# Kernel tuning notes

Measured on AMD Instinct MI355X. Metric: run time of the kernel, lower is better.

Reference implementation:

```python
import jax, jax.numpy as jnp
import numpy as np

N = 50000   # nodes
E = 800000  # random edges (self-loops appended inside reference, as PyG GATConv does)
H = 4       # attention heads
LEAKY_SLOPE = 0.2
BN_EPS = 1e-5


def setup_inputs() -> dict:
    key = jax.random.key(0)
    ks = jax.random.split(key, 24)
    inp = {
        "x": jax.random.normal(ks[0], (N, 128), jnp.float32),
        "edge_index": jax.random.randint(ks[1], (2, E), 0, N, dtype=jnp.int64),
    }
    # layer dims: (in, out_per_head); concat -> out width = H*out
    dims = [(128, 64), (256, 64), (256, 32)]
    i = 2
    for l, (fin, c) in enumerate(dims, start=1):
        sc = 1.0 / np.sqrt(fin)
        inp[f"W{l}"] = jax.random.normal(ks[i], (fin, H * c), jnp.float32) * sc; i += 1
        inp[f"a_src{l}"] = jax.random.normal(ks[i], (H, c), jnp.float32) * 0.1; i += 1
        inp[f"a_dst{l}"] = jax.random.normal(ks[i], (H, c), jnp.float32) * 0.1; i += 1
        inp[f"b{l}"] = jnp.zeros((H * c,), jnp.float32)
    # batch norm params for the two non-final layers (width = 64*4 = 256)
    for l in (1, 2):
        inp[f"gamma{l}"] = jnp.ones((256,), jnp.float32)
        inp[f"beta{l}"] = jnp.zeros((256,), jnp.float32)
    return inp


def _gat_layer(x, src, dst, W, a_src, a_dst, b, heads):
    n = x.shape[0]
    h = (x @ W).reshape(n, heads, -1)                      # [N,H,C]
    al_s = jnp.sum(h * a_src, axis=-1)                     # [N,H]
    al_d = jnp.sum(h * a_dst, axis=-1)                     # [N,H]
    e = jax.nn.leaky_relu(al_s[src] + al_d[dst], LEAKY_SLOPE)  # [Etot,H]
    # numerically-stable edge softmax over incoming edges per destination
    m = jax.ops.segment_max(e, dst, num_segments=n)
    e = jnp.exp(e - m[dst])
    s = jax.ops.segment_sum(e, dst, num_segments=n)
    alpha = e / (s[dst] + 1e-16)                           # [Etot,H]
    msg = alpha[:, :, None] * h[src]                       # [Etot,H,C]
    out = jax.ops.segment_sum(msg, dst, num_segments=n)    # [N,H,C]
    out = out.reshape(n, -1) + b
    return jax.nn.relu(out)  # GAT_NET applies relu after conv


def _batch_norm(x, gamma, beta):
    mean = jnp.mean(x, axis=0)
    var = jnp.var(x, axis=0)  # biased, matches torch BN training normalization
    return (x - mean) * jax.lax.rsqrt(var + BN_EPS) * gamma + beta


def reference(x, edge_index, W1, a_src1, a_dst1, b1, gamma1, beta1,
              W2, a_src2, a_dst2, b2, gamma2, beta2,
              W3, a_src3, a_dst3, b3):
    n = x.shape[0]
    loop = jnp.arange(n, dtype=edge_index.dtype)
    src = jnp.concatenate([edge_index[0], loop])  # add self-loops (PyG default)
    dst = jnp.concatenate([edge_index[1], loop])

    h = _gat_layer(x, src, dst, W1, a_src1, a_dst1, b1, H)
    # outer F.relu is a no-op after GAT_NET's internal relu, kept implicitly
    h = _batch_norm(h, gamma1, beta1)

    h = _gat_layer(h, src, dst, W2, a_src2, a_dst2, b2, H)
    h = _batch_norm(h, gamma2, beta2)

    return _gat_layer(h, src, dst, W3, a_src3, a_dst3, b3, H)
```

## Files before the change

kernel.cpp:

```cpp
#include <hip/hip_runtime.h>
#include <hip/hip_bf16.h>

constexpr int NN   = 50000;
constexpr int EE   = 800000;
constexpr int ETOT = EE + NN;
constexpr int NP   = 50048;
constexpr int NBLK = (NN + 255) / 256;
constexpr float SLOPE  = 0.2f;
constexpr float EPS_BN = 1e-5f;

typedef __attribute__((ext_vector_type(8))) short bf16x8;
typedef __attribute__((ext_vector_type(4))) float f32x4;

__device__ inline float bf2f(unsigned short u) {
    union { unsigned int i; float f; } c; c.i = ((unsigned int)u) << 16; return c.f;
}

__device__ inline void gload16(const __hip_bfloat16* g, __hip_bfloat16* l) {
    __builtin_amdgcn_global_load_lds(
        (const __attribute__((address_space(1))) unsigned int*)g,
        (__attribute__((address_space(3))) unsigned int*)l, 16, 0, 0);
}


__global__ __launch_bounds__(256) void count_kernel(const int* __restrict__ ei,
                                                    int* __restrict__ cnt) {
    int j = blockIdx.x * 256 + threadIdx.x;
    if (j >= ETOT) return;
    int dst = (j < EE) ? ei[EE + j] : (j - EE);
    atomicAdd(&cnt[dst], 1);
}

__global__ __launch_bounds__(256) void scanA_kernel(const int* __restrict__ cnt,
                                                    int* __restrict__ off,
                                                    int* __restrict__ bsum) {
    int b = blockIdx.x, t = threadIdx.x;
    int i = b * 256 + t;
    int v = (i < NN) ? cnt[i] : 0;
    int lane = t & 63, w = t >> 6;
    int x = v;
    #pragma unroll
    for (int o = 1; o < 64; o <<= 1) { int y = __shfl_up(x, o); if (lane >= o) x += y; }
    __shared__ int ws[4];
    if (lane == 63) ws[w] = x;
    __syncthreads();
    int wo = 0;
    for (int k = 0; k < w; ++k) wo += ws[k];
    int incl = x + wo;
    if (i < NN) off[i] = incl - v;
    if (t == 255) bsum[b] = incl;
}

__global__ __launch_bounds__(256) void scanB_kernel(const int* __restrict__ bsum,
                                                    int* __restrict__ bexc,
                                                    int* __restrict__ off) {
    int t = threadIdx.x;
    int v = (t < NBLK) ? bsum[t] : 0;
    int lane = t & 63, w = t >> 6;
    int x = v;
    #pragma unroll
    for (int o = 1; o < 64; o <<= 1) { int y = __shfl_up(x, o); if (lane >= o) x += y; }
    __shared__ int ws[4];
    if (lane == 63) ws[w] = x;
    __syncthreads();
    int wo = 0;
    for (int k = 0; k < w; ++k) wo += ws[k];
    int incl = x + wo;
    if (t < NBLK) bexc[t] = incl - v;
    if (t == 255) off[NN] = incl;
}

__global__ __launch_bounds__(256) void scanC_kernel(const int* __restrict__ bexc,
                                                    int* __restrict__ off,
                                                    int* __restrict__ cur) {
    int i = blockIdx.x * 256 + threadIdx.x;
    if (i >= NN) return;
    int v = off[i] + bexc[blockIdx.x];
    off[i] = v;
    cur[i] = v;
}

__global__ __launch_bounds__(256) void fill_kernel(const int* __restrict__ ei,
                                                   int* __restrict__ cursor,
                                                   int* __restrict__ ssrc) {
    int j = blockIdx.x * 256 + threadIdx.x;
    if (j >= ETOT) return;
    int src, dst;
    if (j < EE) { src = ei[j]; dst = ei[EE + j]; }
    else        { src = dst = j - EE; }
    int pos = atomicAdd(&cursor[dst], 1);
    ssrc[pos] = src;
}

__global__ __launch_bounds__(256) void castx_kernel(const float* __restrict__ X,
                                                    __hip_bfloat16* __restrict__ Xbf) {
    long e0 = ((long)blockIdx.x * 256 + threadIdx.x) * 8;
    if (e0 >= (long)NP * 128) return;
    int row = (int)(e0 / 128);
    __hip_bfloat16 o[8];
    if (row < NN) {
        float4 v0 = *reinterpret_cast<const float4*>(X + e0);
        float4 v1 = *reinterpret_cast<const float4*>(X + e0 + 4);
        o[0] = __float2bfloat16(v0.x); o[1] = __float2bfloat16(v0.y);
        o[2] = __float2bfloat16(v0.z); o[3] = __float2bfloat16(v0.w);
        o[4] = __float2bfloat16(v1.x); o[5] = __float2bfloat16(v1.y);
        o[6] = __float2bfloat16(v1.z); o[7] = __float2bfloat16(v1.w);
    } else {
        for (int j = 0; j < 8; ++j) o[j] = __float2bfloat16(0.f);
    }
    *reinterpret_cast<bf16x8*>(Xbf + e0) = *reinterpret_cast<bf16x8*>(o);
}

__global__ __launch_bounds__(256) void castw1_kernel(const float* __restrict__ W,
                                                     __hip_bfloat16* __restrict__ WT) {
    int i = blockIdx.x * 256 + threadIdx.x;
    if (i >= 32768) return;
    int c = i / 128, k = i % 128;
    WT[i] = __float2bfloat16(W[(size_t)k * 256 + c]);
}

template <int FIN, int WOUT>
__global__ __launch_bounds__(FIN) void foldw_kernel(const float* __restrict__ W,
                                                    const float* __restrict__ scale,
                                                    const float* __restrict__ shift,
                                                    __hip_bfloat16* __restrict__ WTp,
                                                    float* __restrict__ bb) {
    int c = blockIdx.x, k = threadIdx.x;
    float w = W[(size_t)k * WOUT + c];
    WTp[(size_t)c * FIN + k] = __float2bfloat16(scale[k] * w);
    float p = shift[k] * w;
    #pragma unroll
    for (int o = 1; o < 64; o <<= 1) p += __shfl_xor(p, o);
    __shared__ float ps[FIN / 64];
    if ((k & 63) == 0) ps[k >> 6] = p;
    __syncthreads();
    if (k == 0) {
        float s = 0.f;
        #pragma unroll
        for (int q = 0; q < FIN / 64; ++q) s += ps[q];
        bb[c] = s;
    }
}

template <int FIN, int WOUT, bool FOLD>
__global__ __launch_bounds__(256) void mgemm_kernel(const __hip_bfloat16* __restrict__ A,
                                                    const __hip_bfloat16* __restrict__ BT,
                                                    const float* __restrict__ bb,
                                                    const float* __restrict__ a_src,
                                                    const float* __restrict__ a_dst,
                                                    __hip_bfloat16* __restrict__ Hbf,
                                                    float* __restrict__ als,
                                                    float* __restrict__ ald) {
    __shared__ __hip_bfloat16 As[128 * 32];
    __shared__ __hip_bfloat16 Bs[128 * 32];
    int t = threadIdx.x;
    int lane = t & 63, w = t >> 6;
    int row0 = blockIdx.x * 128;
    int col0 = blockIdx.y * 128;
    int wr = w >> 1, wc = w & 1;

    f32x4 acc[4][4];
    #pragma unroll
    for (int m = 0; m < 4; ++m)
        #pragma unroll
        for (int n = 0; n < 4; ++n) acc[m][n] = (f32x4){0.f, 0.f, 0.f, 0.f};

    int srow = w * 32 + (lane >> 2);
    int sbc  = (lane & 3) * 8;
    const __hip_bfloat16* gA0 = A  + (size_t)(row0 + srow)      * FIN + sbc;
    const __hip_bfloat16* gA1 = A  + (size_t)(row0 + srow + 16) * FIN + sbc;
    const __hip_bfloat16* gB0 = BT + (size_t)(col0 + srow)      * FIN + sbc;
    const __hip_bfloat16* gB1 = BT + (size_t)(col0 + srow + 16) * FIN + sbc;
    __hip_bfloat16* lA0 = As + w * 1024;
    __hip_bfloat16* lA1 = As + w * 1024 + 512;
    __hip_bfloat16* lB0 = Bs + w * 1024;
    __hip_bfloat16* lB1 = Bs + w * 1024 + 512;

    int rA = (wr * 64 + (lane & 15)) * 32 + (lane >> 4) * 8;
    int rB = (wc * 64 + (lane & 15)) * 32 + (lane >> 4) * 8;

    for (int k0 = 0; k0 < FIN; k0 += 32) {
        gload16(gA0 + k0, lA0);
        gload16(gA1 + k0, lA1);
        gload16(gB0 + k0, lB0);
        gload16(gB1 + k0, lB1);
        __syncthreads();
        bf16x8 af[4], bfr[4];
        #pragma unroll
        for (int m = 0; m < 4; ++m) af[m]  = *reinterpret_cast<const bf16x8*>(As + rA + m * 16 * 32);
        #pragma unroll
        for (int n = 0; n < 4; ++n) bfr[n] = *reinterpret_cast<const bf16x8*>(Bs + rB + n * 16 * 32);
        #pragma unroll
        for (int m = 0; m < 4; ++m)
            #pragma unroll
            for (int n = 0; n < 4; ++n)
                acc[m][n] = __builtin_amdgcn_mfma_f32_16x16x32_bf16(af[m], bfr[n], acc[m][n], 0, 0, 0);
        __syncthreads();
    }

    int cih = lane & 15;

    if constexpr (FOLD) {
        #pragma unroll
        for (int n = 0; n < 4; ++n) {
            float badd = bb[col0 + wc * 64 + n * 16 + cih];
            #pragma unroll
            for (int m = 0; m < 4; ++m)
                #pragma unroll
                for (int j = 0; j < 4; ++j) acc[m][n][j] += badd;
        }
    }

    float asv[4], adv[4];
    int headw = 0;
    if constexpr (WOUT == 256) {
        headw = (col0 >> 6) + wc;
        #pragma unroll
        for (int n = 0; n < 4; ++n) {
            asv[n] = a_src[headw * 64 + n * 16 + cih];
            adv[n] = a_dst[headw * 64 + n * 16 + cih];
        }
    } else {
        #pragma unroll
        for (int n = 0; n < 4; ++n) {
            int hh = wc * 2 + (n >> 1);
            asv[n] = a_src[hh * 32 + (n & 1) * 16 + cih];
            adv[n] = a_dst[hh * 32 + (n & 1) * 16 + cih];
        }
    }

    #pragma unroll
    for (int m = 0; m < 4; ++m) {
        #pragma unroll
        for (int j = 0; j < 4; ++j) {
            int r = row0 + wr * 64 + m * 16 + (lane >> 4) * 4 + j;
            if constexpr (WOUT == 256) {
                float vs = acc[m][0][j] * asv[0] + acc[m][1][j] * asv[1]
                         + acc[m][2][j] * asv[2] + acc[m][3][j] * asv[3];
                float vd = acc[m][0][j] * adv[0] + acc[m][1][j] * adv[1]
                         + acc[m][2][j] * adv[2] + acc[m][3][j] * adv[3];
                #pragma unroll
                for (int o = 1; o < 16; o <<= 1) {
                    vs += __shfl_xor(vs, o);
                    vd += __shfl_xor(vd, o);
                }
                if (cih == 0) {
                    als[(size_t)r * 4 + headw] = vs;
                    ald[(size_t)r * 4 + headw] = vd;
                }
            } else {
                float vs0 = acc[m][0][j] * asv[0] + acc[m][1][j] * asv[1];
                float vs1 = acc[m][2][j] * asv[2] + acc[m][3][j] * asv[3];
                float vd0 = acc[m][0][j] * adv[0] + acc[m][1][j] * adv[1];
                float vd1 = acc[m][2][j] * adv[2] + acc[m][3][j] * adv[3];
                #pragma unroll
                for (int o = 1; o < 16; o <<= 1) {
                    vs0 += __shfl_xor(vs0, o); vs1 += __shfl_xor(vs1, o);
                    vd0 += __shfl_xor(vd0, o); vd1 += __shfl_xor(vd1, o);
                }
                if (cih == 0) {
                    als[(size_t)r * 4 + wc * 2]     = vs0;
                    als[(size_t)r * 4 + wc * 2 + 1] = vs1;
                    ald[(size_t)r * 4 + wc * 2]     = vd0;
                    ald[(size_t)r * 4 + wc * 2 + 1] = vd1;
                }
            }
        }
    }

    #pragma unroll
    for (int n = 0; n < 4; ++n) {
        int c = col0 + wc * 64 + n * 16 + cih;
        #pragma unroll
        for (int m = 0; m < 4; ++m) {
            int r = row0 + wr * 64 + m * 16 + (lane >> 4) * 4;
            #pragma unroll
            for (int j = 0; j < 4; ++j)
                Hbf[(size_t)(r + j) * WOUT + c] = __float2bfloat16(acc[m][n][j]);
        }
    }
}

template <int HC, bool OUTBF>
__global__ __launch_bounds__(256) void attn_kernel(const __hip_bfloat16* __restrict__ Hm,
                                                   const int* __restrict__ off,
                                                   const int* __restrict__ ssrc,
                                                   const float* __restrict__ als,
                                                   const float* __restrict__ ald,
                                                   const float* __restrict__ bias,
                                                   void* __restrict__ Outv) {
    constexpr int CPL = HC / 16;
    int wid  = threadIdx.x >> 6;
    int lane = threadIdx.x & 63;
    int g    = lane >> 4;
    int q    = lane & 15;
    int d    = blockIdx.x * 16 + wid * 4 + g;
    int head = q >> 2;

    int e0 = off[d], e1 = off[d + 1];
    float aldh = ald[(size_t)d * 4 + head];

    float acc[CPL];
    #pragma unroll
    for (int c = 0; c < CPL; ++c) acc[c] = 0.f;
    float den = 0.f;

    int j = e0;
    for (; j + 3 < e1; j += 4) {
        int s0 = ssrc[j], s1 = ssrc[j + 1], s2 = ssrc[j + 2], s3 = ssrc[j + 3];
        float x0 = als[(size_t)s0 * 4 + head] + aldh;
        float x1 = als[(size_t)s1 * 4 + head] + aldh;
        float x2 = als[(size_t)s2 * 4 + head] + aldh;
        float x3 = als[(size_t)s3 * 4 + head] + aldh;
        x0 = (x0 > 0.f) ? x0 : SLOPE * x0;
        x1 = (x1 > 0.f) ? x1 : SLOPE * x1;
        x2 = (x2 > 0.f) ? x2 : SLOPE * x2;
        x3 = (x3 > 0.f) ? x3 : SLOPE * x3;
        float w0 = __expf(x0), w1 = __expf(x1), w2 = __expf(x2), w3 = __expf(x3);
        den += (w0 + w1) + (w2 + w3);
        const __hip_bfloat16* p0 = Hm + (size_t)s0 * HC + q * CPL;
        const __hip_bfloat16* p1 = Hm + (size_t)s1 * HC + q * CPL;
        const __hip_bfloat16* p2 = Hm + (size_t)s2 * HC + q * CPL;
        const __hip_bfloat16* p3 = Hm + (size_t)s3 * HC + q * CPL;
        if constexpr (CPL == 16) {
            bf16x8 a0 = *reinterpret_cast<const bf16x8*>(p0);
            bf16x8 a1 = *reinterpret_cast<const bf16x8*>(p0 + 8);
            bf16x8 b0 = *reinterpret_cast<const bf16x8*>(p1);
            bf16x8 b1 = *reinterpret_cast<const bf16x8*>(p1 + 8);
            bf16x8 c0 = *reinterpret_cast<const bf16x8*>(p2);
            bf16x8 c1 = *reinterpret_cast<const bf16x8*>(p2 + 8);
            bf16x8 d0 = *reinterpret_cast<const bf16x8*>(p3);
            bf16x8 d1 = *reinterpret_cast<const bf16x8*>(p3 + 8);
            #pragma unroll
            for (int c = 0; c < 8; ++c) {
                acc[c]     += w0 * bf2f((unsigned short)a0[c]) + w1 * bf2f((unsigned short)b0[c])
                            + w2 * bf2f((unsigned short)c0[c]) + w3 * bf2f((unsigned short)d0[c]);
                acc[8 + c] += w0 * bf2f((unsigned short)a1[c]) + w1 * bf2f((unsigned short)b1[c])
                            + w2 * bf2f((unsigned short)c1[c]) + w3 * bf2f((unsigned short)d1[c]);
            }
        } else {
            bf16x8 a0 = *reinterpret_cast<const bf16x8*>(p0);
            bf16x8 b0 = *reinterpret_cast<const bf16x8*>(p1);
            bf16x8 c0 = *reinterpret_cast<const bf16x8*>(p2);
            bf16x8 d0 = *reinterpret_cast<const bf16x8*>(p3);
            #pragma unroll
            for (int c = 0; c < 8; ++c)
                acc[c] += w0 * bf2f((unsigned short)a0[c]) + w1 * bf2f((unsigned short)b0[c])
                        + w2 * bf2f((unsigned short)c0[c]) + w3 * bf2f((unsigned short)d0[c]);
        }
    }
    for (; j < e1; ++j) {
        int s0 = ssrc[j];
        float x0 = als[(size_t)s0 * 4 + head] + aldh;
        x0 = (x0 > 0.f) ? x0 : SLOPE * x0;
        float w0 = __expf(x0);
        den += w0;
        const __hip_bfloat16* p0 = Hm + (size_t)s0 * HC + q * CPL;
        if constexpr (CPL == 16) {
            bf16x8 a0 = *reinterpret_cast<const bf16x8*>(p0);
            bf16x8 a1 = *reinterpret_cast<const bf16x8*>(p0 + 8);
            #pragma unroll
            for (int c = 0; c < 8; ++c) {
                acc[c]     += w0 * bf2f((unsigned short)a0[c]);
                acc[8 + c] += w0 * bf2f((unsigned short)a1[c]);
            }
        } else {
            bf16x8 a0 = *reinterpret_cast<const bf16x8*>(p0);
            #pragma unroll
            for (int c = 0; c < 8; ++c) acc[c] += w0 * bf2f((unsigned short)a0[c]);
        }
    }

    float inv = 1.f / (den + 1e-16f);

    float o[CPL];
    #pragma unroll
    for (int c4 = 0; c4 < CPL / 4; ++c4) {
        float4 b4 = *reinterpret_cast<const float4*>(bias + q * CPL + c4 * 4);
        o[c4 * 4 + 0] = fmaxf(acc[c4 * 4 + 0] * inv + b4.x, 0.f);
        o[c4 * 4 + 1] = fmaxf(acc[c4 * 4 + 1] * inv + b4.y, 0.f);
        o[c4 * 4 + 2] = fmaxf(acc[c4 * 4 + 2] * inv + b4.z, 0.f);
        o[c4 * 4 + 3] = fmaxf(acc[c4 * 4 + 3] * inv + b4.w, 0.f);
    }
    if constexpr (OUTBF) {
        __hip_bfloat16 ob[CPL];
        #pragma unroll
        for (int c = 0; c < CPL; ++c) ob[c] = __float2bfloat16(o[c]);
        __hip_bfloat16* op = (__hip_bfloat16*)Outv + (size_t)d * HC + q * CPL;
        #pragma unroll
        for (int c8 = 0; c8 < CPL / 8; ++c8)
            *reinterpret_cast<bf16x8*>(op + c8 * 8) = *reinterpret_cast<bf16x8*>(ob + c8 * 8);
    } else {
        float* op = (float*)Outv + (size_t)d * HC + q * CPL;
        #pragma unroll
        for (int c4 = 0; c4 < CPL / 4; ++c4)
            *reinterpret_cast<float4*>(op + c4 * 4) =
                make_float4(o[c4*4+0], o[c4*4+1], o[c4*4+2], o[c4*4+3]);
    }
}

__global__ __launch_bounds__(256) void bnstats_kernel(const __hip_bfloat16* __restrict__ X,
                                                      float* __restrict__ sums) {
    int c  = threadIdx.x;
    int r0 = blockIdx.x * 200;
    float s = 0.f, q = 0.f;
    for (int r = r0; r < r0 + 200; ++r) {
        float v = bf2f(*(const unsigned short*)(X + (size_t)r * 256 + c));
        s += v; q += v * v;
    }
    atomicAdd(&sums[c], s);
    atomicAdd(&sums[256 + c], q);
}

__global__ __launch_bounds__(256) void bnfinal_kernel(const float* __restrict__ sums,
                                                      const float* __restrict__ gamma,
                                                      const float* __restrict__ beta,
                                                      float* __restrict__ scale,
                                                      float* __restrict__ shift) {
    int c = threadIdx.x;
    float mean = sums[c] / (float)NN;
    float var  = sums[256 + c] / (float)NN - mean * mean;
    float inv  = rsqrtf(var + EPS_BN);
    float sc   = gamma[c] * inv;
    scale[c] = sc;
    shift[c] = beta[c] - mean * sc;
}


extern "C" void kernel_launch(void* const* d_in, const int* in_sizes, int n_in,
                              void* d_out, int out_size, void* d_ws, size_t ws_size,
                              hipStream_t stream) {
    const float* x      = (const float*)d_in[0];
    const int*   ei     = (const int*)d_in[1];
    const float* W1     = (const float*)d_in[2];
    const float* a_s1   = (const float*)d_in[3];
    const float* a_d1   = (const float*)d_in[4];
    const float* b1     = (const float*)d_in[5];
    const float* W2     = (const float*)d_in[6];
    const float* a_s2   = (const float*)d_in[7];
    const float* a_d2   = (const float*)d_in[8];
    const float* b2     = (const float*)d_in[9];
    const float* W3     = (const float*)d_in[10];
    const float* a_s3   = (const float*)d_in[11];
    const float* a_d3   = (const float*)d_in[12];
    const float* b3     = (const float*)d_in[13];
    const float* gamma1 = (const float*)d_in[14];
    const float* beta1  = (const float*)d_in[15];
    const float* gamma2 = (const float*)d_in[16];
    const float* beta2  = (const float*)d_in[17];

    char* ws = (char*)d_ws;
    size_t o = 0;
    auto alloc = [&](size_t bytes) -> void* {
        void* p = ws + o;
        o = (o + bytes + 255) & ~size_t(255);
        return p;
    };
    __hip_bfloat16*  Abf  = (__hip_bfloat16*)alloc((size_t)NP * 256 * 2);
    __hip_bfloat16*  Hbf  = (__hip_bfloat16*)alloc((size_t)NP * 256 * 2);
    __hip_bfloat16*  Xbf  = (__hip_bfloat16*)alloc((size_t)NP * 128 * 2);
    __hip_bfloat16*  WT1  = (__hip_bfloat16*)alloc((size_t)256 * 128 * 2);
    __hip_bfloat16*  WT2  = (__hip_bfloat16*)alloc((size_t)256 * 256 * 2);
    __hip_bfloat16*  WT3  = (__hip_bfloat16*)alloc((size_t)128 * 256 * 2);
    float* bb2   = (float*)alloc(256 * 4);
    float* bb3   = (float*)alloc(128 * 4);
    float* als   = (float*)alloc((size_t)NP * 4 * 4);
    float* ald   = (float*)alloc((size_t)NP * 4 * 4);
    float* sums  = (float*)alloc(512 * 4);
    float* scale = (float*)alloc(256 * 4);
    float* shift = (float*)alloc(256 * 4);
    int*   off   = (int*)alloc((size_t)(NN + 1) * 4);
    int*   cur   = (int*)alloc((size_t)NN * 4);
    int*   cnt   = (int*)alloc((size_t)NN * 4);
    int*   bsum  = (int*)alloc((size_t)NBLK * 4);
    int*   bexc  = (int*)alloc((size_t)NBLK * 4);
    int*   ssrc  = (int*)alloc((size_t)ETOT * 4);
    (void)ws_size; (void)in_sizes; (void)n_in; (void)out_size;

    const int EB = (ETOT + 255) / 256;

    hipMemsetAsync(cnt, 0, (size_t)NN * 4, stream);
    count_kernel<<<EB, 256, 0, stream>>>(ei, cnt);
    scanA_kernel<<<NBLK, 256, 0, stream>>>(cnt, off, bsum);
    scanB_kernel<<<1, 256, 0, stream>>>(bsum, bexc, off);
    scanC_kernel<<<NBLK, 256, 0, stream>>>(bexc, off, cur);
    fill_kernel<<<EB, 256, 0, stream>>>(ei, cur, ssrc);

    castw1_kernel<<<128, 256, 0, stream>>>(W1, WT1);
    castx_kernel<<<(int)(((long)NP * 128 / 8 + 255) / 256), 256, 0, stream>>>(x, Xbf);
    mgemm_kernel<128, 256, false><<<dim3(NP / 128, 2), 256, 0, stream>>>(
        Xbf, WT1, nullptr, a_s1, a_d1, Hbf, als, ald);
    attn_kernel<256, true><<<NN / 16, 256, 0, stream>>>(Hbf, off, ssrc, als, ald, b1, Abf);

    hipMemsetAsync(sums, 0, 512 * 4, stream);
    bnstats_kernel<<<250, 256, 0, stream>>>(Abf, sums);
    bnfinal_kernel<<<1, 256, 0, stream>>>(sums, gamma1, beta1, scale, shift);
    foldw_kernel<256, 256><<<256, 256, 0, stream>>>(W2, scale, shift, WT2, bb2);

    mgemm_kernel<256, 256, true><<<dim3(NP / 128, 2), 256, 0, stream>>>(
        Abf, WT2, bb2, a_s2, a_d2, Hbf, als, ald);
    attn_kernel<256, true><<<NN / 16, 256, 0, stream>>>(Hbf, off, ssrc, als, ald, b2, Abf);

    hipMemsetAsync(sums, 0, 512 * 4, stream);
    bnstats_kernel<<<250, 256, 0, stream>>>(Abf, sums);
    bnfinal_kernel<<<1, 256, 0, stream>>>(sums, gamma2, beta2, scale, shift);
    foldw_kernel<256, 128><<<128, 256, 0, stream>>>(W3, scale, shift, WT3, bb3);

    mgemm_kernel<256, 128, true><<<dim3(NP / 128, 1), 256, 0, stream>>>(
        Abf, WT3, bb3, a_s3, a_d3, Hbf, als, ald);
    attn_kernel<128, false><<<NN / 16, 256, 0, stream>>>(Hbf, off, ssrc, als, ald, b3, d_out);
}
```

Before: 385.0 us.

## Merge cast and BN-finalize kernels, remap 256-wide attention lanes for coalescing

```diff
diff --git a/kernel.cpp b/kernel.cpp
--- a/kernel.cpp
+++ b/kernel.cpp
@@ -92,54 +92,57 @@
     ssrc[pos] = src;
 }
 
-__global__ __launch_bounds__(256) void castx_kernel(const float* __restrict__ X,
-                                                    __hip_bfloat16* __restrict__ Xbf) {
-    long e0 = ((long)blockIdx.x * 256 + threadIdx.x) * 8;
-    if (e0 >= (long)NP * 128) return;
-    int row = (int)(e0 / 128);
-    __hip_bfloat16 o[8];
-    if (row < NN) {
-        float4 v0 = *reinterpret_cast<const float4*>(X + e0);
-        float4 v1 = *reinterpret_cast<const float4*>(X + e0 + 4);
-        o[0] = __float2bfloat16(v0.x); o[1] = __float2bfloat16(v0.y);
-        o[2] = __float2bfloat16(v0.z); o[3] = __float2bfloat16(v0.w);
-        o[4] = __float2bfloat16(v1.x); o[5] = __float2bfloat16(v1.y);
-        o[6] = __float2bfloat16(v1.z); o[7] = __float2bfloat16(v1.w);
+constexpr int XB = (int)(((long)NP * 128 / 8 + 255) / 256);
+__global__ __launch_bounds__(256) void castwx_kernel(const float* __restrict__ X,
+                                                     const float* __restrict__ W,
+                                                     __hip_bfloat16* __restrict__ Xbf,
+                                                     __hip_bfloat16* __restrict__ WT) {
+    int b = blockIdx.x;
+    if (b < XB) {
+        long e0 = ((long)b * 256 + threadIdx.x) * 8;
+        if (e0 >= (long)NP * 128) return;
+        int row = (int)(e0 / 128);
+        __hip_bfloat16 o[8];
+        if (row < NN) {
+            float4 v0 = *reinterpret_cast<const float4*>(X + e0);
+            float4 v1 = *reinterpret_cast<const float4*>(X + e0 + 4);
+            o[0] = __float2bfloat16(v0.x); o[1] = __float2bfloat16(v0.y);
+            o[2] = __float2bfloat16(v0.z); o[3] = __float2bfloat16(v0.w);
+            o[4] = __float2bfloat16(v1.x); o[5] = __float2bfloat16(v1.y);
+            o[6] = __float2bfloat16(v1.z); o[7] = __float2bfloat16(v1.w);
+        } else {
+            for (int j = 0; j < 8; ++j) o[j] = __float2bfloat16(0.f);
+        }
+        *reinterpret_cast<bf16x8*>(Xbf + e0) = *reinterpret_cast<bf16x8*>(o);
     } else {
-        for (int j = 0; j < 8; ++j) o[j] = __float2bfloat16(0.f);
-    }
-    *reinterpret_cast<bf16x8*>(Xbf + e0) = *reinterpret_cast<bf16x8*>(o);
-}
-
-__global__ __launch_bounds__(256) void castw1_kernel(const float* __restrict__ W,
-                                                     __hip_bfloat16* __restrict__ WT) {
-    int i = blockIdx.x * 256 + threadIdx.x;
-    if (i >= 32768) return;
-    int c = i / 128, k = i % 128;
-    WT[i] = __float2bfloat16(W[(size_t)k * 256 + c]);
-}
-
-template <int FIN, int WOUT>
-__global__ __launch_bounds__(FIN) void foldw_kernel(const float* __restrict__ W,
-                                                    const float* __restrict__ scale,
-                                                    const float* __restrict__ shift,
+        int i = (b - XB) * 256 + threadIdx.x;
+        int c = i / 128, k = i % 128;
+        WT[i] = __float2bfloat16(W[(size_t)k * 256 + c]);
+    }
+}
+
+template <int WOUT>
+__global__ __launch_bounds__(256) void foldw_kernel(const float* __restrict__ W,
+                                                    const float* __restrict__ sums,
+                                                    const float* __restrict__ gamma,
+                                                    const float* __restrict__ beta,
                                                     __hip_bfloat16* __restrict__ WTp,
                                                     float* __restrict__ bb) {
     int c = blockIdx.x, k = threadIdx.x;
+    float mean = sums[k] / (float)NN;
+    float var  = sums[256 + k] / (float)NN - mean * mean;
+    float inv  = rsqrtf(var + EPS_BN);
+    float sc   = gamma[k] * inv;
+    float sh   = beta[k] - mean * sc;
     float w = W[(size_t)k * WOUT + c];
-    WTp[(size_t)c * FIN + k] = __float2bfloat16(scale[k] * w);
-    float p = shift[k] * w;
+    WTp[(size_t)c * 256 + k] = __float2bfloat16(sc * w);
+    float p = sh * w;
     #pragma unroll
     for (int o = 1; o < 64; o <<= 1) p += __shfl_xor(p, o);
-    __shared__ float ps[FIN / 64];
+    __shared__ float ps[4];
     if ((k & 63) == 0) ps[k >> 6] = p;
     __syncthreads();
-    if (k == 0) {
-        float s = 0.f;
-        #pragma unroll
-        for (int q = 0; q < FIN / 64; ++q) s += ps[q];
-        bb[c] = s;
-    }
+    if (k == 0) bb[c] = ps[0] + ps[1] + ps[2] + ps[3];
 }
 
 template <int FIN, int WOUT, bool FOLD>
@@ -281,15 +284,118 @@
     }
 }
 
-template <int HC, bool OUTBF>
-__global__ __launch_bounds__(256) void attn_kernel(const __hip_bfloat16* __restrict__ Hm,
-                                                   const int* __restrict__ off,
-                                                   const int* __restrict__ ssrc,
-                                                   const float* __restrict__ als,
-                                                   const float* __restrict__ ald,
-                                                   const float* __restrict__ bias,
-                                                   void* __restrict__ Outv) {
-    constexpr int CPL = HC / 16;
+__global__ __launch_bounds__(256) void attn256_kernel(const __hip_bfloat16* __restrict__ Hm,
+                                                      const int* __restrict__ off,
+                                                      const int* __restrict__ ssrc,
+                                                      const float* __restrict__ als,
+                                                      const float* __restrict__ ald,
+                                                      const float* __restrict__ bias,
+                                                      __hip_bfloat16* __restrict__ Out) {
+    int wid  = threadIdx.x >> 6;
+    int lane = threadIdx.x & 63;
+    int g    = lane >> 4;
+    int q    = lane & 15;
+    int d    = blockIdx.x * 16 + wid * 4 + g;
+    int hA   = q >> 3;
+
+    int e0 = off[d], e1 = off[d + 1];
+    float aldA = ald[(size_t)d * 4 + hA];
+    float aldB = ald[(size_t)d * 4 + hA + 2];
+
+    float accA[8], accB[8];
+    #pragma unroll
+    for (int c = 0; c < 8; ++c) { accA[c] = 0.f; accB[c] = 0.f; }
+    float denA = 0.f, denB = 0.f;
+
+    int j = e0;
+    for (; j + 3 < e1; j += 4) {
+        int s0 = ssrc[j], s1 = ssrc[j + 1], s2 = ssrc[j + 2], s3 = ssrc[j + 3];
+        const __hip_bfloat16* r0 = Hm + (size_t)s0 * 256 + q * 8;
+        const __hip_bfloat16* r1 = Hm + (size_t)s1 * 256 + q * 8;
+        const __hip_bfloat16* r2 = Hm + (size_t)s2 * 256 + q * 8;
+        const __hip_bfloat16* r3 = Hm + (size_t)s3 * 256 + q * 8;
+        bf16x8 a0 = *reinterpret_cast<const bf16x8*>(r0);
+        bf16x8 b0 = *reinterpret_cast<const bf16x8*>(r0 + 128);
+        bf16x8 a1 = *reinterpret_cast<const bf16x8*>(r1);
+        bf16x8 b1 = *reinterpret_cast<const bf16x8*>(r1 + 128);
+        bf16x8 a2 = *reinterpret_cast<const bf16x8*>(r2);
+        bf16x8 b2 = *reinterpret_cast<const bf16x8*>(r2 + 128);
+        bf16x8 a3 = *reinterpret_cast<const bf16x8*>(r3);
+        bf16x8 b3 = *reinterpret_cast<const bf16x8*>(r3 + 128);
+        float xA0 = als[(size_t)s0 * 4 + hA] + aldA, xB0 = als[(size_t)s0 * 4 + hA + 2] + aldB;
+        float xA1 = als[(size_t)s1 * 4 + hA] + aldA, xB1 = als[(size_t)s1 * 4 + hA + 2] + aldB;
+        float xA2 = als[(size_t)s2 * 4 + hA] + aldA, xB2 = als[(size_t)s2 * 4 + hA + 2] + aldB;
+        float xA3 = als[(size_t)s3 * 4 + hA] + aldA, xB3 = als[(size_t)s3 * 4 + hA + 2] + aldB;
+        xA0 = (xA0 > 0.f) ? xA0 : SLOPE * xA0;  xB0 = (xB0 > 0.f) ? xB0 : SLOPE * xB0;
+        xA1 = (xA1 > 0.f) ? xA1 : SLOPE * xA1;  xB1 = (xB1 > 0.f) ? xB1 : SLOPE * xB1;
+        xA2 = (xA2 > 0.f) ? xA2 : SLOPE * xA2;  xB2 = (xB2 > 0.f) ? xB2 : SLOPE * xB2;
+        xA3 = (xA3 > 0.f) ? xA3 : SLOPE * xA3;  xB3 = (xB3 > 0.f) ? xB3 : SLOPE * xB3;
+        float wA0 = __expf(xA0), wB0 = __expf(xB0);
+        float wA1 = __expf(xA1), wB1 = __expf(xB1);
+        float wA2 = __expf(xA2), wB2 = __expf(xB2);
+        float wA3 = __expf(xA3), wB3 = __expf(xB3);
+        denA += (wA0 + wA1) + (wA2 + wA3);
+        denB += (wB0 + wB1) + (wB2 + wB3);
+        #pragma unroll
+        for (int c = 0; c < 8; ++c) {
+            accA[c] += wA0 * bf2f((unsigned short)a0[c]) + wA1 * bf2f((unsigned short)a1[c])
+                     + wA2 * bf2f((unsigned short)a2[c]) + wA3 * bf2f((unsigned short)a3[c]);
+            accB[c] += wB0 * bf2f((unsigned short)b0[c]) + wB1 * bf2f((unsigned short)b1[c])
+                     + wB2 * bf2f((unsigned short)b2[c]) + wB3 * bf2f((unsigned short)b3[c]);
+        }
+    }
+    for (; j < e1; ++j) {
+        int s0 = ssrc[j];
+        const __hip_bfloat16* r0 = Hm + (size_t)s0 * 256 + q * 8;
+        bf16x8 a0 = *reinterpret_cast<const bf16x8*>(r0);
+        bf16x8 b0 = *reinterpret_cast<const bf16x8*>(r0 + 128);
+        float xA0 = als[(size_t)s0 * 4 + hA] + aldA, xB0 = als[(size_t)s0 * 4 + hA + 2] + aldB;
+        xA0 = (xA0 > 0.f) ? xA0 : SLOPE * xA0;  xB0 = (xB0 > 0.f) ? xB0 : SLOPE * xB0;
+        float wA0 = __expf(xA0), wB0 = __expf(xB0);
+        denA += wA0; denB += wB0;
+        #pragma unroll
+        for (int c = 0; c < 8; ++c) {
+            accA[c] += wA0 * bf2f((unsigned short)a0[c]);
+            accB[c] += wB0 * bf2f((unsigned short)b0[c]);
+        }
+    }
+
+    float invA = 1.f / (denA + 1e-16f);
+    float invB = 1.f / (denB + 1e-16f);
+
+    float4 bA0 = *reinterpret_cast<const float4*>(bias + q * 8);
+    float4 bA1 = *reinterpret_cast<const float4*>(bias + q * 8 + 4);
+    float4 bB0 = *reinterpret_cast<const float4*>(bias + 128 + q * 8);
+    float4 bB1 = *reinterpret_cast<const float4*>(bias + 128 + q * 8 + 4);
+    __hip_bfloat16 oA[8], oB[8];
+    oA[0] = __float2bfloat16(fmaxf(accA[0] * invA + bA0.x, 0.f));
+    oA[1] = __float2bfloat16(fmaxf(accA[1] * invA + bA0.y, 0.f));
+    oA[2] = __float2bfloat16(fmaxf(accA[2] * invA + bA0.z, 0.f));
+    oA[3] = __float2bfloat16(fmaxf(accA[3] * invA + bA0.w, 0.f));
+    oA[4] = __float2bfloat16(fmaxf(accA[4] * invA + bA1.x, 0.f));
+    oA[5] = __float2bfloat16(fmaxf(accA[5] * invA + bA1.y, 0.f));
+    oA[6] = __float2bfloat16(fmaxf(accA[6] * invA + bA1.z, 0.f));
+    oA[7] = __float2bfloat16(fmaxf(accA[7] * invA + bA1.w, 0.f));
+    oB[0] = __float2bfloat16(fmaxf(accB[0] * invB + bB0.x, 0.f));
+    oB[1] = __float2bfloat16(fmaxf(accB[1] * invB + bB0.y, 0.f));
+    oB[2] = __float2bfloat16(fmaxf(accB[2] * invB + bB0.z, 0.f));
+    oB[3] = __float2bfloat16(fmaxf(accB[3] * invB + bB0.w, 0.f));
+    oB[4] = __float2bfloat16(fmaxf(accB[4] * invB + bB1.x, 0.f));
+    oB[5] = __float2bfloat16(fmaxf(accB[5] * invB + bB1.y, 0.f));
+    oB[6] = __float2bfloat16(fmaxf(accB[6] * invB + bB1.z, 0.f));
+    oB[7] = __float2bfloat16(fmaxf(accB[7] * invB + bB1.w, 0.f));
+    __hip_bfloat16* op = Out + (size_t)d * 256 + q * 8;
+    *reinterpret_cast<bf16x8*>(op)       = *reinterpret_cast<bf16x8*>(oA);
+    *reinterpret_cast<bf16x8*>(op + 128) = *reinterpret_cast<bf16x8*>(oB);
+}
+
+__global__ __launch_bounds__(256) void attn128_kernel(const __hip_bfloat16* __restrict__ Hm,
+                                                      const int* __restrict__ off,
+                                                      const int* __restrict__ ssrc,
+                                                      const float* __restrict__ als,
+                                                      const float* __restrict__ ald,
+                                                      const float* __restrict__ bias,
+                                                      float* __restrict__ Out) {
     int wid  = threadIdx.x >> 6;
     int lane = threadIdx.x & 63;
     int g    = lane >> 4;
@@ -300,14 +406,18 @@
     int e0 = off[d], e1 = off[d + 1];
     float aldh = ald[(size_t)d * 4 + head];
 
-    float acc[CPL];
-    #pragma unroll
-    for (int c = 0; c < CPL; ++c) acc[c] = 0.f;
+    float acc[8];
+    #pragma unroll
+    for (int c = 0; c < 8; ++c) acc[c] = 0.f;
     float den = 0.f;
 
     int j = e0;
     for (; j + 3 < e1; j += 4) {
         int s0 = ssrc[j], s1 = ssrc[j + 1], s2 = ssrc[j + 2], s3 = ssrc[j + 3];
+        bf16x8 a0 = *reinterpret_cast<const bf16x8*>(Hm + (size_t)s0 * 128 + q * 8);
+        bf16x8 a1 = *reinterpret_cast<const bf16x8*>(Hm + (size_t)s1 * 128 + q * 8);
+        bf16x8 a2 = *reinterpret_cast<const bf16x8*>(Hm + (size_t)s2 * 128 + q * 8);
+        bf16x8 a3 = *reinterpret_cast<const bf16x8*>(Hm + (size_t)s3 * 128 + q * 8);
         float x0 = als[(size_t)s0 * 4 + head] + aldh;
         float x1 = als[(size_t)s1 * 4 + head] + aldh;
         float x2 = als[(size_t)s2 * 4 + head] + aldh;
@@ -318,85 +428,32 @@
         x3 = (x3 > 0.f) ? x3 : SLOPE * x3;
         float w0 = __expf(x0), w1 = __expf(x1), w2 = __expf(x2), w3 = __expf(x3);
         den += (w0 + w1) + (w2 + w3);
-        const __hip_bfloat16* p0 = Hm + (size_t)s0 * HC + q * CPL;
-        const __hip_bfloat16* p1 = Hm + (size_t)s1 * HC + q * CPL;
-        const __hip_bfloat16* p2 = Hm + (size_t)s2 * HC + q * CPL;
-        const __hip_bfloat16* p3 = Hm + (size_t)s3 * HC + q * CPL;
-        if constexpr (CPL == 16) {
-            bf16x8 a0 = *reinterpret_cast<const bf16x8*>(p0);
-            bf16x8 a1 = *reinterpret_cast<const bf16x8*>(p0 + 8);
-            bf16x8 b0 = *reinterpret_cast<const bf16x8*>(p1);
-            bf16x8 b1 = *reinterpret_cast<const bf16x8*>(p1 + 8);
-            bf16x8 c0 = *reinterpret_cast<const bf16x8*>(p2);
-            bf16x8 c1 = *reinterpret_cast<const bf16x8*>(p2 + 8);
-            bf16x8 d0 = *reinterpret_cast<const bf16x8*>(p3);
-            bf16x8 d1 = *reinterpret_cast<const bf16x8*>(p3 + 8);
-            #pragma unroll
-            for (int c = 0; c < 8; ++c) {
-                acc[c]     += w0 * bf2f((unsigned short)a0[c]) + w1 * bf2f((unsigned short)b0[c])
-                            + w2 * bf2f((unsigned short)c0[c]) + w3 * bf2f((unsigned short)d0[c]);
-                acc[8 + c] += w0 * bf2f((unsigned short)a1[c]) + w1 * bf2f((unsigned short)b1[c])
-                            + w2 * bf2f((unsigned short)c1[c]) + w3 * bf2f((unsigned short)d1[c]);
-            }
-        } else {
-            bf16x8 a0 = *reinterpret_cast<const bf16x8*>(p0);
-            bf16x8 b0 = *reinterpret_cast<const bf16x8*>(p1);
-            bf16x8 c0 = *reinterpret_cast<const bf16x8*>(p2);
-            bf16x8 d0 = *reinterpret_cast<const bf16x8*>(p3);
-            #pragma unroll
-            for (int c = 0; c < 8; ++c)
-                acc[c] += w0 * bf2f((unsigned short)a0[c]) + w1 * bf2f((unsigned short)b0[c])
-                        + w2 * bf2f((unsigned short)c0[c]) + w3 * bf2f((unsigned short)d0[c]);
-        }
+        #pragma unroll
+        for (int c = 0; c < 8; ++c)
+            acc[c] += w0 * bf2f((unsigned short)a0[c]) + w1 * bf2f((unsigned short)a1[c])
+                    + w2 * bf2f((unsigned short)a2[c]) + w3 * bf2f((unsigned short)a3[c]);
     }
     for (; j < e1; ++j) {
         int s0 = ssrc[j];
+        bf16x8 a0 = *reinterpret_cast<const bf16x8*>(Hm + (size_t)s0 * 128 + q * 8);
         float x0 = als[(size_t)s0 * 4 + head] + aldh;
         x0 = (x0 > 0.f) ? x0 : SLOPE * x0;
         float w0 = __expf(x0);
         den += w0;
-        const __hip_bfloat16* p0 = Hm + (size_t)s0 * HC + q * CPL;
-        if constexpr (CPL == 16) {
-            bf16x8 a0 = *reinterpret_cast<const bf16x8*>(p0);
-            bf16x8 a1 = *reinterpret_cast<const bf16x8*>(p0 + 8);
-            #pragma unroll
-            for (int c = 0; c < 8; ++c) {
-                acc[c]     += w0 * bf2f((unsigned short)a0[c]);
-                acc[8 + c] += w0 * bf2f((unsigned short)a1[c]);
-            }
-        } else {
-            bf16x8 a0 = *reinterpret_cast<const bf16x8*>(p0);
-            #pragma unroll
-            for (int c = 0; c < 8; ++c) acc[c] += w0 * bf2f((unsigned short)a0[c]);
-        }
+        #pragma unroll
+        for (int c = 0; c < 8; ++c) acc[c] += w0 * bf2f((unsigned short)a0[c]);
     }
 
     float inv = 1.f / (den + 1e-16f);
-
-    float o[CPL];
-    #pragma unroll
-    for (int c4 = 0; c4 < CPL / 4; ++c4) {
-        float4 b4 = *reinterpret_cast<const float4*>(bias + q * CPL + c4 * 4);
-        o[c4 * 4 + 0] = fmaxf(acc[c4 * 4 + 0] * inv + b4.x, 0.f);
-        o[c4 * 4 + 1] = fmaxf(acc[c4 * 4 + 1] * inv + b4.y, 0.f);
-        o[c4 * 4 + 2] = fmaxf(acc[c4 * 4 + 2] * inv + b4.z, 0.f);
-        o[c4 * 4 + 3] = fmaxf(acc[c4 * 4 + 3] * inv + b4.w, 0.f);
-    }
-    if constexpr (OUTBF) {
-        __hip_bfloat16 ob[CPL];
-        #pragma unroll
-        for (int c = 0; c < CPL; ++c) ob[c] = __float2bfloat16(o[c]);
-        __hip_bfloat16* op = (__hip_bfloat16*)Outv + (size_t)d * HC + q * CPL;
-        #pragma unroll
-        for (int c8 = 0; c8 < CPL / 8; ++c8)
-            *reinterpret_cast<bf16x8*>(op + c8 * 8) = *reinterpret_cast<bf16x8*>(ob + c8 * 8);
-    } else {
-        float* op = (float*)Outv + (size_t)d * HC + q * CPL;
-        #pragma unroll
-        for (int c4 = 0; c4 < CPL / 4; ++c4)
-            *reinterpret_cast<float4*>(op + c4 * 4) =
-                make_float4(o[c4*4+0], o[c4*4+1], o[c4*4+2], o[c4*4+3]);
-    }
+    float4 b0 = *reinterpret_cast<const float4*>(bias + q * 8);
+    float4 b1 = *reinterpret_cast<const float4*>(bias + q * 8 + 4);
+    float* op = Out + (size_t)d * 128 + q * 8;
+    *reinterpret_cast<float4*>(op) = make_float4(
+        fmaxf(acc[0] * inv + b0.x, 0.f), fmaxf(acc[1] * inv + b0.y, 0.f),
+        fmaxf(acc[2] * inv + b0.z, 0.f), fmaxf(acc[3] * inv + b0.w, 0.f));
+    *reinterpret_cast<float4*>(op + 4) = make_float4(
+        fmaxf(acc[4] * inv + b1.x, 0.f), fmaxf(acc[5] * inv + b1.y, 0.f),
+        fmaxf(acc[6] * inv + b1.z, 0.f), fmaxf(acc[7] * inv + b1.w, 0.f));
 }
 
 __global__ __launch_bounds__(256) void bnstats_kernel(const __hip_bfloat16* __restrict__ X,
@@ -410,20 +467,6 @@
     }
     atomicAdd(&sums[c], s);
     atomicAdd(&sums[256 + c], q);
-}
-
-__global__ __launch_bounds__(256) void bnfinal_kernel(const float* __restrict__ sums,
-                                                      const float* __restrict__ gamma,
-                                                      const float* __restrict__ beta,
-                                                      float* __restrict__ scale,
-                                                      float* __restrict__ shift) {
-    int c = threadIdx.x;
-    float mean = sums[c] / (float)NN;
-    float var  = sums[256 + c] / (float)NN - mean * mean;
-    float inv  = rsqrtf(var + EPS_BN);
-    float sc   = gamma[c] * inv;
-    scale[c] = sc;
-    shift[c] = beta[c] - mean * sc;
 }
 
 
@@ -467,8 +510,6 @@
     float* als   = (float*)alloc((size_t)NP * 4 * 4);
     float* ald   = (float*)alloc((size_t)NP * 4 * 4);
     float* sums  = (float*)alloc(512 * 4);
-    float* scale = (float*)alloc(256 * 4);
-    float* shift = (float*)alloc(256 * 4);
     int*   off   = (int*)alloc((size_t)(NN + 1) * 4);
     int*   cur   = (int*)alloc((size_t)NN * 4);
     int*   cnt   = (int*)alloc((size_t)NN * 4);
@@ -486,27 +527,24 @@
     scanC_kernel<<<NBLK, 256, 0, stream>>>(bexc, off, cur);
     fill_kernel<<<EB, 256, 0, stream>>>(ei, cur, ssrc);
 
-    castw1_kernel<<<128, 256, 0, stream>>>(W1, WT1);
-    castx_kernel<<<(int)(((long)NP * 128 / 8 + 255) / 256), 256, 0, stream>>>(x, Xbf);
+    castwx_kernel<<<XB + 128, 256, 0, stream>>>(x, W1, Xbf, WT1);
     mgemm_kernel<128, 256, false><<<dim3(NP / 128, 2), 256, 0, stream>>>(
         Xbf, WT1, nullptr, a_s1, a_d1, Hbf, als, ald);
-    attn_kernel<256, true><<<NN / 16, 256, 0, stream>>>(Hbf, off, ssrc, als, ald, b1, Abf);
+    attn256_kernel<<<NN / 16, 256, 0, stream>>>(Hbf, off, ssrc, als, ald, b1, Abf);
 
     hipMemsetAsync(sums, 0, 512 * 4, stream);
     bnstats_kernel<<<250, 256, 0, stream>>>(Abf, sums);
-    bnfinal_kernel<<<1, 256, 0, stream>>>(sums, gamma1, beta1, scale, shift);
-    foldw_kernel<256, 256><<<256, 256, 0, stream>>>(W2, scale, shift, WT2, bb2);
+    foldw_kernel<256><<<256, 256, 0, stream>>>(W2, sums, gamma1, beta1, WT2, bb2);
 
     mgemm_kernel<256, 256, true><<<dim3(NP / 128, 2), 256, 0, stream>>>(
         Abf, WT2, bb2, a_s2, a_d2, Hbf, als, ald);
-    attn_kernel<256, true><<<NN / 16, 256, 0, stream>>>(Hbf, off, ssrc, als, ald, b2, Abf);
+    attn256_kernel<<<NN / 16, 256, 0, stream>>>(Hbf, off, ssrc, als, ald, b2, Abf);
 
     hipMemsetAsync(sums, 0, 512 * 4, stream);
     bnstats_kernel<<<250, 256, 0, stream>>>(Abf, sums);
-    bnfinal_kernel<<<1, 256, 0, stream>>>(sums, gamma2, beta2, scale, shift);
-    foldw_kernel<256, 128><<<128, 256, 0, stream>>>(W3, scale, shift, WT3, bb3);
+    foldw_kernel<128><<<128, 256, 0, stream>>>(W3, sums, gamma2, beta2, WT3, bb3);
 
     mgemm_kernel<256, 128, true><<<dim3(NP / 128, 1), 256, 0, stream>>>(
         Abf, WT3, bb3, a_s3, a_d3, Hbf, als, ald);
-    attn_kernel<128, false><<<NN / 16, 256, 0, stream>>>(Hbf, off, ssrc, als, ald, b3, d_out);
-}
+    attn128_kernel<<<NN / 16, 256, 0, stream>>>(Hbf, off, ssrc, als, ald, b3, (float*)d_out);
+}
```

New measurement: 382.1 us. About the same (-0.7%).
